# Kernel optimization log

Hardware: AMD Instinct MI355X
Metric: run time of the kernel (lower is better)

The kernel has to match this reference:

```python
import jax, jax.numpy as jnp
import numpy as np

NCLASS = 1000
H = 1.0
MIN_EPS = 1e-10
IGNORE_INDEX = -100


def setup_inputs() -> dict:
    key = jax.random.key(0)
    k1, k2, k3, k4 = jax.random.split(key, 4)
    N, M, D = 16384, 4096, 256
    return {
        "supp_embed": jax.random.normal(k1, (N, D), dtype=jnp.float32),
        "pred_embed": jax.random.normal(k2, (M, D), dtype=jnp.float32),
        "supp_target": jax.random.randint(k3, (N,), 0, NCLASS, dtype=jnp.int64)
        if jax.config.jax_enable_x64 else jax.random.randint(k3, (N,), 0, NCLASS, dtype=jnp.int32),
        "target": jax.random.randint(k4, (M,), 0, NCLASS, dtype=jnp.int32),
    }


def _kde_ce(supp_embed, pred_embed, supp_target, target):
    d = supp_embed.shape[1]
    sq = (jnp.sum(pred_embed * pred_embed, axis=1, keepdims=True)
          + jnp.sum(supp_embed * supp_embed, axis=1)[None, :]
          - 2.0 * pred_embed @ supp_embed.T)
    sq = jnp.maximum(sq, 0.0)
    K = jnp.exp(sq / (-d * H))                      # RBF kernel, (M, N)
    # drop_max is False here (X_pred provided, not LOO); weights = 1.0
    K = K / jnp.clip(jnp.sum(K, axis=1, keepdims=True), MIN_EPS)
    Y = jax.nn.one_hot(supp_target, NCLASS, dtype=K.dtype)  # (N, K)
    pred = K @ Y                                    # class probabilities (M, K)
    # LogLoss: NLL on probabilities with ignore_index + mean reduction
    valid = target != IGNORE_INDEX
    safe_t = jnp.where(valid, target, 0)
    p = jnp.take_along_axis(pred, safe_t[:, None], axis=1)[:, 0]
    nll = -jnp.log(jnp.clip(p, MIN_EPS))
    loss = jnp.sum(nll * valid) / jnp.maximum(jnp.sum(valid), 1)
    return loss, pred


def reference(supp_embed, pred_embed, supp_target, target):
    loss, pred = _kde_ce(supp_embed, pred_embed, supp_target, target)
    return loss
```

## Files before the change

### kernel.cpp

```cpp
#include <hip/hip_runtime.h>
#include <hip/hip_bf16.h>

typedef __bf16 bf16x8 __attribute__((ext_vector_type(8)));
typedef float  f32x4  __attribute__((ext_vector_type(4)));
typedef short  short8 __attribute__((ext_vector_type(8)));
typedef unsigned int u32;

#define KDE_IGNORE (-100)
#define NSL  16
#define GBM  64
#define GBN  64
#define BK   128
#define GD   256
#define NSLOT (NSL * 2)

__device__ __forceinline__ f32x4 mfma16x16(bf16x8 a, bf16x8 b, f32x4 c) {
  return __builtin_amdgcn_mfma_f32_16x16x32_bf16(a, b, c, 0, 0, 0);
}

__device__ __forceinline__ void gload_lds16(const short* g, short* l) {
  __builtin_amdgcn_global_load_lds(
      (const __attribute__((address_space(1))) u32*)g,
      (__attribute__((address_space(3))) u32*)l, 16, 0, 0);
}

__device__ __forceinline__ bf16x8 cvt8b(const float* p) {
  float4 a = *reinterpret_cast<const float4*>(p);
  float4 b = *reinterpret_cast<const float4*>(p + 4);
  union { bf16x8 v; __bf16 h[8]; } u;
  u.h[0] = (__bf16)a.x; u.h[1] = (__bf16)a.y; u.h[2] = (__bf16)a.z; u.h[3] = (__bf16)a.w;
  u.h[4] = (__bf16)b.x; u.h[5] = (__bf16)b.y; u.h[6] = (__bf16)b.z; u.h[7] = (__bf16)b.w;
  return u.v;
}
__device__ __forceinline__ short8 cvt8s(const float* p) {
  union { bf16x8 b; short8 s; } u; u.b = cvt8b(p); return u.s;
}

template<bool CONV>
__global__ void supp_prep_kernel(const float* __restrict__ supp, float* __restrict__ sn,
                                 short* __restrict__ suppB, int N) {
  int row = blockIdx.x * 8 + ((threadIdx.x >> 6) << 1) + ((threadIdx.x & 63) >> 5);
  int c = threadIdx.x & 31;
  const float* src = supp + (size_t)row * GD + c * 8;
  float4 a = *reinterpret_cast<const float4*>(src);
  float4 b = *reinterpret_cast<const float4*>(src + 4);
  if (CONV) {
    union { short8 v; __bf16 h[8]; } u;
    u.h[0] = (__bf16)a.x; u.h[1] = (__bf16)a.y; u.h[2] = (__bf16)a.z; u.h[3] = (__bf16)a.w;
    u.h[4] = (__bf16)b.x; u.h[5] = (__bf16)b.y; u.h[6] = (__bf16)b.z; u.h[7] = (__bf16)b.w;
    int h = c >> 4, j = c & 15;
    int pos = h * 16 + (j ^ (row & 15));
    *reinterpret_cast<short8*>(suppB + (size_t)row * GD + pos * 8) = u.v;
  }
  float s = a.x*a.x + a.y*a.y + a.z*a.z + a.w*a.w
          + b.x*b.x + b.y*b.y + b.z*b.z + b.w*b.w;
#pragma unroll
  for (int off = 16; off >= 1; off >>= 1) s += __shfl_xor(s, off, 32);
  if (c == 0) sn[row] = s;
}

template<bool PRE>
__global__ __launch_bounds__(256, 3)
void kde_gemm_kernel(const float* __restrict__ pred, const float* __restrict__ suppF,
                     const short* __restrict__ suppB,
                     const int* __restrict__ tgt, const int* __restrict__ suppT,
                     const float* __restrict__ sn,
                     float* __restrict__ denomP, float* __restrict__ numerP,
                     int M, int N) {
  __shared__ __align__(16) short Bs[2][GBN * BK];

  const int bid = blockIdx.x;
  const int mb  = bid >> 4;
  const int s   = bid & 15;
  const int m0  = mb * GBM;
  const int nslice = N >> 4;
  const int nbase  = s * nslice;
  const int ntile  = nslice / GBN;
  const int t    = threadIdx.x;
  const int lane = t & 63;
  const int wid  = t >> 6;
  const int wm   = (wid >> 1) * 32;
  const int wng  = wid & 1;
  const int wnl  = wng * 32;
  const int lr = lane >> 4, lc = lane & 15;

  const int gvoff = (lane >> 4) * GD + (lane & 15) * 8;

  bf16x8 af[2][8];
#pragma unroll
  for (int mt = 0; mt < 2; ++mt) {
    const float* base = pred + (size_t)(m0 + wm + mt * 16 + lc) * GD + lr * 8;
#pragma unroll
    for (int kk = 0; kk < 8; ++kk) af[mt][kk] = cvt8b(base + kk * 32);
  }
  int tmv[2][4];
#pragma unroll
  for (int mt = 0; mt < 2; ++mt)
#pragma unroll
    for (int rg = 0; rg < 4; ++rg)
      tmv[mt][rg] = tgt[m0 + wm + mt * 16 + lr * 4 + rg];

  float dac[2][4] = {}, nac[2][4] = {};

  const float SC  = 1.4426950408889634f / 128.0f;
  const float SCH = 1.4426950408889634f / 256.0f;

  if (PRE) {
#pragma unroll
    for (int i = 0; i < 4; ++i) {
      int rowbase = wid * 16 + i * 4;
      gload_lds16(suppB + (size_t)(nbase + rowbase) * GD + gvoff, &Bs[0][rowbase * BK]);
    }
  } else {
#pragma unroll
    for (int i = 0; i < 4; ++i) {
      int C = i * 256 + t; int row = C >> 4; int j = C & 15;
      short8 v = cvt8s(suppF + (size_t)(nbase + row) * GD + j * 8);
      *reinterpret_cast<short8*>(&Bs[0][row * BK + ((j ^ (row & 15)) << 3)]) = v;
    }
  }
  __syncthreads();

  f32x4 acc[2][2] = {};
  float snv[2]; int stv[2];
#pragma unroll
  for (int nt = 0; nt < 2; ++nt) {
    int j = nbase + wnl + nt * 16 + lc;
    snv[nt] = sn[j]; stv[nt] = suppT[j];
  }

  for (int it = 0; it < ntile; ++it) {
    const int n0 = nbase + it * GBN;
    const bool more = (it + 1 < ntile);

    short8 sreg[4];
    if (PRE) {
#pragma unroll
      for (int i = 0; i < 4; ++i) {
        int rowbase = wid * 16 + i * 4;
        gload_lds16(suppB + (size_t)(n0 + rowbase) * GD + BK + gvoff, &Bs[1][rowbase * BK]);
      }
    } else {
#pragma unroll
      for (int i = 0; i < 4; ++i) {
        int C = i * 256 + t; int row = C >> 4; int j = C & 15;
        sreg[i] = cvt8s(suppF + (size_t)(n0 + row) * GD + BK + j * 8);
      }
    }
    __builtin_amdgcn_s_setprio(1);
#pragma unroll
    for (int ks = 0; ks < 4; ++ks) {
      bf16x8 bfr[2];
#pragma unroll
      for (int nt = 0; nt < 2; ++nt) {
        int r = wnl + nt * 16 + lc;
        int cs = (ks * 4 + lr) ^ (r & 15);
        bfr[nt] = *reinterpret_cast<const bf16x8*>(&Bs[0][r * BK + (cs << 3)]);
      }
#pragma unroll
      for (int mt = 0; mt < 2; ++mt)
#pragma unroll
        for (int nt = 0; nt < 2; ++nt)
          acc[mt][nt] = mfma16x16(af[mt][ks], bfr[nt], acc[mt][nt]);
    }
    __builtin_amdgcn_s_setprio(0);
    if (!PRE) {
#pragma unroll
      for (int i = 0; i < 4; ++i) {
        int C = i * 256 + t; int row = C >> 4; int j = C & 15;
        *reinterpret_cast<short8*>(&Bs[1][row * BK + ((j ^ (row & 15)) << 3)]) = sreg[i];
      }
    }
    __syncthreads();

    if (more) {
      if (PRE) {
#pragma unroll
        for (int i = 0; i < 4; ++i) {
          int rowbase = wid * 16 + i * 4;
          gload_lds16(suppB + (size_t)(n0 + GBN + rowbase) * GD + gvoff, &Bs[0][rowbase * BK]);
        }
      } else {
#pragma unroll
        for (int i = 0; i < 4; ++i) {
          int C = i * 256 + t; int row = C >> 4; int j = C & 15;
          sreg[i] = cvt8s(suppF + (size_t)(n0 + GBN + row) * GD + j * 8);
        }
      }
    }
    __builtin_amdgcn_s_setprio(1);
#pragma unroll
    for (int ks = 0; ks < 4; ++ks) {
      bf16x8 bfr[2];
#pragma unroll
      for (int nt = 0; nt < 2; ++nt) {
        int r = wnl + nt * 16 + lc;
        int cs = (ks * 4 + lr) ^ (r & 15);
        bfr[nt] = *reinterpret_cast<const bf16x8*>(&Bs[1][r * BK + (cs << 3)]);
      }
#pragma unroll
      for (int mt = 0; mt < 2; ++mt)
#pragma unroll
        for (int nt = 0; nt < 2; ++nt)
          acc[mt][nt] = mfma16x16(af[mt][4 + ks], bfr[nt], acc[mt][nt]);
    }
    __builtin_amdgcn_s_setprio(0);
    if (!PRE && more) {
#pragma unroll
      for (int i = 0; i < 4; ++i) {
        int C = i * 256 + t; int row = C >> 4; int j = C & 15;
        *reinterpret_cast<short8*>(&Bs[0][row * BK + ((j ^ (row & 15)) << 3)]) = sreg[i];
      }
    }

#pragma unroll
    for (int nt = 0; nt < 2; ++nt) {
      float sh = -snv[nt] * SCH;
#pragma unroll
      for (int mt = 0; mt < 2; ++mt)
#pragma unroll
        for (int rg = 0; rg < 4; ++rg) {
          float e = exp2f(fmaf(acc[mt][nt][rg], SC, sh));
          dac[mt][rg] += e;
          nac[mt][rg] += (stv[nt] == tmv[mt][rg]) ? e : 0.0f;
        }
    }
#pragma unroll
    for (int mt = 0; mt < 2; ++mt)
#pragma unroll
      for (int nt = 0; nt < 2; ++nt) acc[mt][nt] = f32x4{0.f, 0.f, 0.f, 0.f};
    if (more) {
      const int nn0 = n0 + GBN;
#pragma unroll
      for (int nt = 0; nt < 2; ++nt) {
        int j = nn0 + wnl + nt * 16 + lc;
        snv[nt] = sn[j]; stv[nt] = suppT[j];
      }
    }
    __syncthreads();
  }

#pragma unroll
  for (int off = 1; off < 16; off <<= 1) {
#pragma unroll
    for (int mt = 0; mt < 2; ++mt)
#pragma unroll
      for (int rg = 0; rg < 4; ++rg) {
        dac[mt][rg] += __shfl_xor(dac[mt][rg], off);
        nac[mt][rg] += __shfl_xor(nac[mt][rg], off);
      }
  }
  if (lc == 0) {
    const int slot = s * 2 + wng;
#pragma unroll
    for (int mt = 0; mt < 2; ++mt)
#pragma unroll
      for (int rg = 0; rg < 4; ++rg) {
        int m = m0 + wm + mt * 16 + lr * 4 + rg;
        denomP[(size_t)slot * M + m] = dac[mt][rg];
        numerP[(size_t)slot * M + m] = nac[mt][rg];
      }
  }
}

__global__ void kde_reduce_kernel(const float* __restrict__ denomP, const float* __restrict__ numerP,
                                  const int* __restrict__ tgt,
                                  float* __restrict__ bsum, float* __restrict__ bcnt, int M) {
  __shared__ float sS[4], sC[4];
  int m = blockIdx.x * 256 + threadIdx.x;
  float den = 0.0f, num = 0.0f;
#pragma unroll
  for (int sl = 0; sl < NSLOT; ++sl) {
    den += denomP[(size_t)sl * M + m];
    num += numerP[(size_t)sl * M + m];
  }
  int tg = tgt[m];
  bool valid = (tg != KDE_IGNORE);
  float p = fmaxf(num / fmaxf(den, 1e-10f), 1e-10f);
  float nll = valid ? -logf(p) : 0.0f;
  float cnt = valid ? 1.0f : 0.0f;
#pragma unroll
  for (int off = 32; off >= 1; off >>= 1) {
    nll += __shfl_xor(nll, off);
    cnt += __shfl_xor(cnt, off);
  }
  int wid = threadIdx.x >> 6, lane = threadIdx.x & 63;
  if (lane == 0) { sS[wid] = nll; sC[wid] = cnt; }
  __syncthreads();
  if (threadIdx.x == 0) {
    bsum[blockIdx.x] = sS[0] + sS[1] + sS[2] + sS[3];
    bcnt[blockIdx.x] = sC[0] + sC[1] + sC[2] + sC[3];
  }
}

__global__ void kde_final_kernel(const float* __restrict__ bsum, const float* __restrict__ bcnt,
                                 float* __restrict__ out, int nb) {
  int tid = threadIdx.x;
  float s = (tid < nb) ? bsum[tid] : 0.0f;
  float c = (tid < nb) ? bcnt[tid] : 0.0f;
#pragma unroll
  for (int off = 32; off >= 1; off >>= 1) {
    s += __shfl_xor(s, off);
    c += __shfl_xor(c, off);
  }
  if (tid == 0) out[0] = s / fmaxf(c, 1.0f);
}

extern "C" void kernel_launch(void* const* d_in, const int* in_sizes, int n_in,
                              void* d_out, int out_size, void* d_ws, size_t ws_size,
                              hipStream_t stream) {
  const float* supp  = (const float*)d_in[0];
  const float* pred  = (const float*)d_in[1];
  const int*   suppT = (const int*)d_in[2];
  const int*   tgt   = (const int*)d_in[3];
  const int N = in_sizes[2];
  const int M = in_sizes[3];

  float* sn     = (float*)d_ws;
  float* denomP = sn + N;
  float* numerP = denomP + (size_t)NSLOT * M;
  float* bsum   = numerP + (size_t)NSLOT * M;
  float* bcnt   = bsum + 16;
  short* suppB  = (short*)(bcnt + 16);

  size_t small = sizeof(float) * ((size_t)N + 2 * (size_t)NSLOT * M + 32);
  bool pre = ws_size >= small + sizeof(short) * (size_t)N * GD;

  if (pre) supp_prep_kernel<true ><<<dim3(N / 8), dim3(256), 0, stream>>>(supp, sn, suppB, N);
  else     supp_prep_kernel<false><<<dim3(N / 8), dim3(256), 0, stream>>>(supp, sn, nullptr, N);

  dim3 grid((M / GBM) * NSL);
  if (pre) kde_gemm_kernel<true ><<<grid, dim3(256), 0, stream>>>(
      pred, supp, suppB, tgt, suppT, sn, denomP, numerP, M, N);
  else     kde_gemm_kernel<false><<<grid, dim3(256), 0, stream>>>(
      pred, supp, suppB, tgt, suppT, sn, denomP, numerP, M, N);

  kde_reduce_kernel<<<dim3(M / 256), dim3(256), 0, stream>>>(denomP, numerP, tgt, bsum, bcnt, M);
  kde_final_kernel<<<dim3(1), dim3(64), 0, stream>>>(bsum, bcnt, (float*)d_out, M / 256);
}
```

Measured before the change: 92.10 us.

## Double M tile per block and pre-convert pred embeddings to bf16

Doubles the M tile from 64 to 128 rows, so each wave holds four 16-row A fragments and each B tile staged in LDS feeds twice as many MFMAs. This halves the grid and the total B traffic through global memory and LDS. The prep kernel now also converts pred to bf16, so the GEMM loads A fragments directly instead of converting from fp32. The trade-off is much higher register pressure (launch bounds lowered to 2 blocks per SM), a grid of only 512 blocks for 256 CUs, and volatile loads that may block load coalescing.

```diff
diff --git a/kernel.cpp b/kernel.cpp
--- a/kernel.cpp
+++ b/kernel.cpp
@@ -8,7 +8,7 @@
 
 #define KDE_IGNORE (-100)
 #define NSL  16
-#define GBM  64
+#define GBM  128
 #define GBN  64
 #define BK   128
 #define GD   256
@@ -22,6 +22,13 @@
   __builtin_amdgcn_global_load_lds(
       (const __attribute__((address_space(1))) u32*)g,
       (__attribute__((address_space(3))) u32*)l, 16, 0, 0);
+}
+
+__device__ __forceinline__ bf16x8 vload_bf16x8(const short* p) {
+  union { int v[4]; bf16x8 b; } u;
+  const volatile int* q = reinterpret_cast<const volatile int*>(p);
+  u.v[0] = q[0]; u.v[1] = q[1]; u.v[2] = q[2]; u.v[3] = q[3];
+  return u.b;
 }
 
 __device__ __forceinline__ bf16x8 cvt8b(const float* p) {
@@ -37,32 +44,44 @@
 }
 
 template<bool CONV>
-__global__ void supp_prep_kernel(const float* __restrict__ supp, float* __restrict__ sn,
-                                 short* __restrict__ suppB, int N) {
-  int row = blockIdx.x * 8 + ((threadIdx.x >> 6) << 1) + ((threadIdx.x & 63) >> 5);
-  int c = threadIdx.x & 31;
-  const float* src = supp + (size_t)row * GD + c * 8;
-  float4 a = *reinterpret_cast<const float4*>(src);
-  float4 b = *reinterpret_cast<const float4*>(src + 4);
-  if (CONV) {
-    union { short8 v; __bf16 h[8]; } u;
-    u.h[0] = (__bf16)a.x; u.h[1] = (__bf16)a.y; u.h[2] = (__bf16)a.z; u.h[3] = (__bf16)a.w;
-    u.h[4] = (__bf16)b.x; u.h[5] = (__bf16)b.y; u.h[6] = (__bf16)b.z; u.h[7] = (__bf16)b.w;
-    int h = c >> 4, j = c & 15;
-    int pos = h * 16 + (j ^ (row & 15));
-    *reinterpret_cast<short8*>(suppB + (size_t)row * GD + pos * 8) = u.v;
-  }
-  float s = a.x*a.x + a.y*a.y + a.z*a.z + a.w*a.w
-          + b.x*b.x + b.y*b.y + b.z*b.z + b.w*b.w;
-#pragma unroll
-  for (int off = 16; off >= 1; off >>= 1) s += __shfl_xor(s, off, 32);
-  if (c == 0) sn[row] = s;
+__global__ void prep_kernel(const float* __restrict__ supp, const float* __restrict__ pred,
+                            float* __restrict__ sn, short* __restrict__ suppB,
+                            short* __restrict__ predB, int N, int M) {
+  const int nbS = N >> 3;
+  const int b = blockIdx.x;
+  const int sub = ((threadIdx.x >> 6) << 1) + ((threadIdx.x & 63) >> 5);
+  const int c = threadIdx.x & 31;
+  if (b < nbS) {
+    int row = b * 8 + sub;
+    const float* src = supp + (size_t)row * GD + c * 8;
+    float4 a = *reinterpret_cast<const float4*>(src);
+    float4 v = *reinterpret_cast<const float4*>(src + 4);
+    if (CONV) {
+      union { short8 s8; __bf16 h[8]; } u;
+      u.h[0] = (__bf16)a.x; u.h[1] = (__bf16)a.y; u.h[2] = (__bf16)a.z; u.h[3] = (__bf16)a.w;
+      u.h[4] = (__bf16)v.x; u.h[5] = (__bf16)v.y; u.h[6] = (__bf16)v.z; u.h[7] = (__bf16)v.w;
+      int h = c >> 4, j = c & 15;
+      int pos = h * 16 + (j ^ (row & 15));
+      *reinterpret_cast<short8*>(suppB + (size_t)row * GD + pos * 8) = u.s8;
+    }
+    float s = a.x*a.x + a.y*a.y + a.z*a.z + a.w*a.w
+            + v.x*v.x + v.y*v.y + v.z*v.z + v.w*v.w;
+#pragma unroll
+    for (int off = 16; off >= 1; off >>= 1) s += __shfl_xor(s, off, 32);
+    if (c == 0) sn[row] = s;
+  } else if (CONV) {
+    int row = (b - nbS) * 8 + sub;
+    if (row < M) {
+      const float* src = pred + (size_t)row * GD + c * 8;
+      *reinterpret_cast<short8*>(predB + (size_t)row * GD + c * 8) = cvt8s(src);
+    }
+  }
 }
 
 template<bool PRE>
-__global__ __launch_bounds__(256, 3)
+__global__ __launch_bounds__(256, 2)
 void kde_gemm_kernel(const float* __restrict__ pred, const float* __restrict__ suppF,
-                     const short* __restrict__ suppB,
+                     const short* __restrict__ suppB, const short* __restrict__ predB,
                      const int* __restrict__ tgt, const int* __restrict__ suppT,
                      const float* __restrict__ sn,
                      float* __restrict__ denomP, float* __restrict__ numerP,
@@ -79,28 +98,37 @@
   const int t    = threadIdx.x;
   const int lane = t & 63;
   const int wid  = t >> 6;
-  const int wm   = (wid >> 1) * 32;
+  const int wm   = (wid >> 1) * 64;
   const int wng  = wid & 1;
   const int wnl  = wng * 32;
   const int lr = lane >> 4, lc = lane & 15;
 
   const int gvoff = (lane >> 4) * GD + (lane & 15) * 8;
 
-  bf16x8 af[2][8];
-#pragma unroll
-  for (int mt = 0; mt < 2; ++mt) {
-    const float* base = pred + (size_t)(m0 + wm + mt * 16 + lc) * GD + lr * 8;
-#pragma unroll
-    for (int kk = 0; kk < 8; ++kk) af[mt][kk] = cvt8b(base + kk * 32);
-  }
-  int tmv[2][4];
-#pragma unroll
-  for (int mt = 0; mt < 2; ++mt)
+  bf16x8 af[4][8];
+  if (PRE) {
+    const short* abase = predB + (size_t)(m0 + wm + lc) * GD + lr * 8;
+#pragma unroll
+    for (int mt = 0; mt < 4; ++mt)
+#pragma unroll
+      for (int kk = 0; kk < 8; ++kk)
+        af[mt][kk] = vload_bf16x8(abase + mt * 16 * GD + kk * 32);
+  } else {
+    const float* abaseF = pred + (size_t)(m0 + wm + lc) * GD + lr * 8;
+#pragma unroll
+    for (int mt = 0; mt < 4; ++mt)
+#pragma unroll
+      for (int kk = 0; kk < 8; ++kk)
+        af[mt][kk] = cvt8b(abaseF + mt * 16 * GD + kk * 32);
+  }
+  int tmv[4][4];
+#pragma unroll
+  for (int mt = 0; mt < 4; ++mt)
 #pragma unroll
     for (int rg = 0; rg < 4; ++rg)
       tmv[mt][rg] = tgt[m0 + wm + mt * 16 + lr * 4 + rg];
 
-  float dac[2][4] = {}, nac[2][4] = {};
+  float dac[4][4] = {}, nac[4][4] = {};
 
   const float SC  = 1.4426950408889634f / 128.0f;
   const float SCH = 1.4426950408889634f / 256.0f;
@@ -121,7 +149,7 @@
   }
   __syncthreads();
 
-  f32x4 acc[2][2] = {};
+  f32x4 acc[4][2] = {};
   float snv[2]; int stv[2];
 #pragma unroll
   for (int nt = 0; nt < 2; ++nt) {
@@ -158,7 +186,7 @@
         bfr[nt] = *reinterpret_cast<const bf16x8*>(&Bs[0][r * BK + (cs << 3)]);
       }
 #pragma unroll
-      for (int mt = 0; mt < 2; ++mt)
+      for (int mt = 0; mt < 4; ++mt)
 #pragma unroll
         for (int nt = 0; nt < 2; ++nt)
           acc[mt][nt] = mfma16x16(af[mt][ks], bfr[nt], acc[mt][nt]);
@@ -199,7 +227,7 @@
         bfr[nt] = *reinterpret_cast<const bf16x8*>(&Bs[1][r * BK + (cs << 3)]);
       }
 #pragma unroll
-      for (int mt = 0; mt < 2; ++mt)
+      for (int mt = 0; mt < 4; ++mt)
 #pragma unroll
         for (int nt = 0; nt < 2; ++nt)
           acc[mt][nt] = mfma16x16(af[mt][4 + ks], bfr[nt], acc[mt][nt]);
@@ -217,7 +245,7 @@
     for (int nt = 0; nt < 2; ++nt) {
       float sh = -snv[nt] * SCH;
 #pragma unroll
-      for (int mt = 0; mt < 2; ++mt)
+      for (int mt = 0; mt < 4; ++mt)
 #pragma unroll
         for (int rg = 0; rg < 4; ++rg) {
           float e = exp2f(fmaf(acc[mt][nt][rg], SC, sh));
@@ -226,7 +254,7 @@
         }
     }
 #pragma unroll
-    for (int mt = 0; mt < 2; ++mt)
+    for (int mt = 0; mt < 4; ++mt)
 #pragma unroll
       for (int nt = 0; nt < 2; ++nt) acc[mt][nt] = f32x4{0.f, 0.f, 0.f, 0.f};
     if (more) {
@@ -243,7 +271,7 @@
 #pragma unroll
   for (int off = 1; off < 16; off <<= 1) {
 #pragma unroll
-    for (int mt = 0; mt < 2; ++mt)
+    for (int mt = 0; mt < 4; ++mt)
 #pragma unroll
       for (int rg = 0; rg < 4; ++rg) {
         dac[mt][rg] += __shfl_xor(dac[mt][rg], off);
@@ -253,7 +281,7 @@
   if (lc == 0) {
     const int slot = s * 2 + wng;
 #pragma unroll
-    for (int mt = 0; mt < 2; ++mt)
+    for (int mt = 0; mt < 4; ++mt)
 #pragma unroll
       for (int rg = 0; rg < 4; ++rg) {
         int m = m0 + wm + mt * 16 + lr * 4 + rg;
@@ -322,18 +350,19 @@
   float* bsum   = numerP + (size_t)NSLOT * M;
   float* bcnt   = bsum + 16;
   short* suppB  = (short*)(bcnt + 16);
+  short* predB  = suppB + (size_t)N * GD;
 
   size_t small = sizeof(float) * ((size_t)N + 2 * (size_t)NSLOT * M + 32);
-  bool pre = ws_size >= small + sizeof(short) * (size_t)N * GD;
-
-  if (pre) supp_prep_kernel<true ><<<dim3(N / 8), dim3(256), 0, stream>>>(supp, sn, suppB, N);
-  else     supp_prep_kernel<false><<<dim3(N / 8), dim3(256), 0, stream>>>(supp, sn, nullptr, N);
+  bool pre = ws_size >= small + sizeof(short) * (size_t)(N + M) * GD;
+
+  if (pre) prep_kernel<true ><<<dim3(N / 8 + M / 8), dim3(256), 0, stream>>>(supp, pred, sn, suppB, predB, N, M);
+  else     prep_kernel<false><<<dim3(N / 8), dim3(256), 0, stream>>>(supp, pred, sn, nullptr, nullptr, N, M);
 
   dim3 grid((M / GBM) * NSL);
   if (pre) kde_gemm_kernel<true ><<<grid, dim3(256), 0, stream>>>(
-      pred, supp, suppB, tgt, suppT, sn, denomP, numerP, M, N);
+      pred, supp, suppB, predB, tgt, suppT, sn, denomP, numerP, M, N);
   else     kde_gemm_kernel<false><<<grid, dim3(256), 0, stream>>>(
-      pred, supp, suppB, tgt, suppT, sn, denomP, numerP, M, N);
+      pred, supp, suppB, predB, tgt, suppT, sn, denomP, numerP, M, N);
 
   kde_reduce_kernel<<<dim3(M / 256), dim3(256), 0, stream>>>(denomP, numerP, tgt, bsum, bcnt, M);
   kde_final_kernel<<<dim3(1), dim3(64), 0, stream>>>(bsum, bcnt, (float*)d_out, M / 256);
```

Result: slower. 105.1 us (+14.2%).
